# Kernel optimization log

Hardware: AMD Instinct MI355X
Metric: run time of the kernel (lower is better)

Reference implementation:

```python
import jax, jax.numpy as jnp
import numpy as np


def setup_inputs() -> dict:
    key = jax.random.key(0)
    k1, k2 = jax.random.split(key)
    B, S, H = 8, 2048, 1024
    lstm_output = jax.random.normal(k1, (B, S, H), dtype=jnp.float32)
    # xavier-uniform-like init for the bilinear weight
    limit = float(np.sqrt(6.0 / (H + H)))
    attention_weights = jax.random.uniform(k2, (H, H), dtype=jnp.float32, minval=-limit, maxval=limit)
    return {"lstm_output": lstm_output, "attention_weights": attention_weights}


def reference(lstm_output, attention_weights):
    # scores[b,i,j] = (x[b,i] @ W) . x[b,j]
    xw = jnp.einsum('bsh,hk->bsk', lstm_output, attention_weights)      # [B,S,H]
    scores = jnp.einsum('bsk,btk->bst', xw, lstm_output)                # [B,S,S]
    attn = jax.nn.softmax(scores, axis=-1)                              # [B,S,S]
    context = jnp.einsum('bst,bth->bsh', attn, lstm_output)             # [B,S,H]
    return (context, attn)
```

## Files before the change

kernel.cpp:

```cpp
#include <hip/hip_runtime.h>
#include <hip/hip_bf16.h>


#define BB 8
#define SS 2048
#define HH 1024

typedef __attribute__((ext_vector_type(8))) short bf16x8;
typedef __attribute__((ext_vector_type(4))) float f32x4;

__device__ __forceinline__ void async_load16(const void* gsrc, void* ldst) {
    typedef const unsigned int __attribute__((address_space(1)))* gp_t;
    typedef unsigned int __attribute__((address_space(3)))* lp_t;
    __builtin_amdgcn_global_load_lds((gp_t)gsrc, (lp_t)ldst, 16, 0, 0);
}

__device__ __forceinline__ unsigned short f2b(float f) {
    __hip_bfloat16 h = __float2bfloat16(f);
    return *(unsigned short*)&h;
}
__device__ __forceinline__ float b2f(unsigned short u) {
    __hip_bfloat16 h = *(__hip_bfloat16*)&u;
    return __bfloat162float(h);
}

__global__ __launch_bounds__(256) void split_x(const float* __restrict__ X,
                                               unsigned short* __restrict__ Xh,
                                               unsigned short* __restrict__ Xl) {
    const size_t i = ((size_t)blockIdx.x * 256 + threadIdx.x) * 8;
    float4 a = *(const float4*)(X + i);
    float4 b = *(const float4*)(X + i + 4);
    ushort4 h0, h1, l0, l1;
    float v, hf;
    v = a.x; h0.x = f2b(v); hf = b2f(h0.x); l0.x = f2b(v - hf);
    v = a.y; h0.y = f2b(v); hf = b2f(h0.y); l0.y = f2b(v - hf);
    v = a.z; h0.z = f2b(v); hf = b2f(h0.z); l0.z = f2b(v - hf);
    v = a.w; h0.w = f2b(v); hf = b2f(h0.w); l0.w = f2b(v - hf);
    v = b.x; h1.x = f2b(v); hf = b2f(h1.x); l1.x = f2b(v - hf);
    v = b.y; h1.y = f2b(v); hf = b2f(h1.y); l1.y = f2b(v - hf);
    v = b.z; h1.z = f2b(v); hf = b2f(h1.z); l1.z = f2b(v - hf);
    v = b.w; h1.w = f2b(v); hf = b2f(h1.w); l1.w = f2b(v - hf);
    *(ushort4*)(Xh + i) = h0; *(ushort4*)(Xh + i + 4) = h1;
    *(ushort4*)(Xl + i) = l0; *(ushort4*)(Xl + i + 4) = l1;
}

__global__ __launch_bounds__(256) void split_wT(const float* __restrict__ W,
                                                unsigned short* __restrict__ Th,
                                                unsigned short* __restrict__ Tl) {
    const int k0 = blockIdx.y * 64, n0 = blockIdx.x * 64;
    __shared__ float tile[64][65];
#pragma unroll
    for (int q = 0; q < 16; q++) {
        int idx = q * 256 + threadIdx.x;
        int r = idx >> 6, c = idx & 63;
        tile[r][c] = W[(size_t)(k0 + r) * HH + n0 + c];
    }
    __syncthreads();
#pragma unroll
    for (int q = 0; q < 16; q++) {
        int idx = q * 256 + threadIdx.x;
        int r = idx >> 6, c = idx & 63;
        float v = tile[c][r];
        unsigned short h = f2b(v);
        Th[(size_t)(n0 + r) * HH + k0 + c] = h;
        Tl[(size_t)(n0 + r) * HH + k0 + c] = f2b(v - b2f(h));
    }
}

#define SPLIT3_8P_BODY(A_h, A_l, B_h, B_l)                                          \
    __shared__ __align__(16) unsigned short lds[65536];                             \
    const int tid = threadIdx.x;                                                    \
    const int wave = tid >> 6, lane = tid & 63;                                     \
    const int m16 = lane & 15, quad = lane >> 4;                                    \
    const int wy = wave >> 2, wx = wave & 3;                                        \
    const int rP = tid >> 2;                                                        \
    const int kq = (tid & 3) ^ ((rP >> 1) & 3);                                     \
    const int cs = quad ^ ((m16 >> 1) & 3);                                         \
    const int wt16 = wave * 1024;                                                   \
    const int rowA_off = (rP & 63) + ((rP >> 6) << 7);                              \
    const int rowB_off = ((rP >> 5) << 6) + (rP & 31);                              \
    const size_t aOff = (size_t)(i0 + rowA_off) * HH + kq * 8;                      \
    const size_t bOff = (size_t)(j0 + rowB_off) * HH + kq * 8;                      \
    f32x4 acc[2][4][2][2] = {};                                                     \
    bf16x8 a_h[4], a_l[4], b_h[2][2], b_l[2][2];                                    \
    STG_A(0, 0, 0); STG_A(1, 0, 0);                                                 \
    STG_B(0, 0, 0); STG_B(1, 0, 0);                                                 \
    STG_B(0, 1, 1); STG_B(1, 1, 1);                                                 \
    asm volatile("s_waitcnt vmcnt(4)" ::: "memory");                                \
    __builtin_amdgcn_s_barrier();                                                   \
    RD_A(0, 0); RD_B(0, 0); RD_B(1, 0);                                             \
    for (int kt = 0; kt < 32; ++kt) {                                               \
        const int bufc = kt & 1, bufn = bufc ^ 1;                                   \
        const int ktA = kt < 31 ? kt + 1 : 31;                                      \
        const int ktB = kt < 30 ? kt + 2 : 31;                                      \
                                                            \
        STG_A(0, ktA, bufn);                                                        \
        __builtin_amdgcn_s_barrier();                                               \
        __builtin_amdgcn_sched_barrier(0);                                          \
        MFMA_PH(0, 0)                                                               \
        __builtin_amdgcn_sched_barrier(0);                                          \
        __builtin_amdgcn_s_barrier();                                               \
                                                            \
        asm volatile("s_waitcnt vmcnt(6)" ::: "memory");                            \
        STG_A(1, ktA, bufn);                                                        \
        __builtin_amdgcn_s_barrier();                                               \
        __builtin_amdgcn_sched_barrier(0);                                          \
        MFMA_PH(0, 1)                                                               \
        __builtin_amdgcn_sched_barrier(0);                                          \
        RD_A(1, bufc);                                                              \
        __builtin_amdgcn_s_barrier();                                               \
                                                            \
        asm volatile("s_waitcnt vmcnt(6)" ::: "memory");                            \
        STG_B(0, ktB, bufc);                                                        \
        __builtin_amdgcn_s_barrier();                                               \
        __builtin_amdgcn_sched_barrier(0);                                          \
        MFMA_PH(1, 0)                                                               \
        __builtin_amdgcn_sched_barrier(0);                                          \
        RD_B(0, bufn);                                                              \
        __builtin_amdgcn_s_barrier();                                               \
                                                            \
        asm volatile("s_waitcnt vmcnt(4)" ::: "memory");                            \
        STG_B(1, ktB, bufc);                                                        \
        __builtin_amdgcn_s_barrier();                                               \
        __builtin_amdgcn_sched_barrier(0);                                          \
        MFMA_PH(1, 1)                                                               \
        __builtin_amdgcn_sched_barrier(0);                                          \
        RD_B(1, bufn);                                                              \
        RD_A(0, bufn);                                                              \
        __builtin_amdgcn_s_barrier();                                               \
    }

#define STG_A(mh, kt, buf) do { \
        const size_t o_ = aOff + (size_t)(mh) * 64 * HH + (size_t)(kt) * 32; \
        async_load16(A_h + o_, (char*)lds + ((buf) * 32768 + (mh) * 4096) * 2 + wt16); \
        async_load16(A_l + o_, (char*)lds + ((buf) * 32768 + 8192 + (mh) * 4096) * 2 + wt16); \
    } while (0)
#define STG_B(nh, kt, buf) do { \
        const size_t o_ = bOff + (size_t)(nh) * 32 * HH + (size_t)(kt) * 32; \
        async_load16(B_h + o_, (char*)lds + ((buf) * 32768 + 16384 + (nh) * 4096) * 2 + wt16); \
        async_load16(B_l + o_, (char*)lds + ((buf) * 32768 + 24576 + (nh) * 4096) * 2 + wt16); \
    } while (0)
#define RD_A(mh, buf) do { \
        const int s0_ = (buf) * 32768 + ((mh) * 128 + wy * 64 + m16) * 32 + cs * 8; \
        _Pragma("unroll") for (int mi = 0; mi < 4; ++mi) { \
            a_h[mi] = *(const bf16x8*)&lds[s0_ + mi * 512]; \
            a_l[mi] = *(const bf16x8*)&lds[8192 + s0_ + mi * 512]; \
        } } while (0)
#define RD_B(nh, buf) do { \
        const int s0_ = (buf) * 32768 + ((nh) * 128 + wx * 32 + m16) * 32 + cs * 8; \
        _Pragma("unroll") for (int nj = 0; nj < 2; ++nj) { \
            b_h[nh][nj] = *(const bf16x8*)&lds[16384 + s0_ + nj * 512]; \
            b_l[nh][nj] = *(const bf16x8*)&lds[24576 + s0_ + nj * 512]; \
        } } while (0)
#define MFMA_PH(mh, nh) \
        __builtin_amdgcn_s_setprio(1); \
        _Pragma("unroll") for (int mi = 0; mi < 4; ++mi) \
        _Pragma("unroll") for (int nj = 0; nj < 2; ++nj) { \
            acc[mh][mi][nh][nj] = __builtin_amdgcn_mfma_f32_16x16x32_bf16(a_h[mi], b_h[nh][nj], acc[mh][mi][nh][nj], 0, 0, 0); \
            acc[mh][mi][nh][nj] = __builtin_amdgcn_mfma_f32_16x16x32_bf16(a_h[mi], b_l[nh][nj], acc[mh][mi][nh][nj], 0, 0, 0); \
            acc[mh][mi][nh][nj] = __builtin_amdgcn_mfma_f32_16x16x32_bf16(a_l[mi], b_h[nh][nj], acc[mh][mi][nh][nj], 0, 0, 0); \
        } \
        __builtin_amdgcn_s_setprio(0);

__global__ __launch_bounds__(512, 2) void gemm_xw3_8p(const unsigned short* __restrict__ Ah,
                                                      const unsigned short* __restrict__ Al,
                                                      const unsigned short* __restrict__ Bh,
                                                      const unsigned short* __restrict__ Bl,
                                                      unsigned short* __restrict__ Ch,
                                                      unsigned short* __restrict__ Cl) {
    const int b = blockIdx.z;
    const int i0 = blockIdx.y * 256, j0 = blockIdx.x * 256;
    const unsigned short* A_h = Ah + (size_t)b * SS * HH;
    const unsigned short* A_l = Al + (size_t)b * SS * HH;
    const unsigned short* B_h = Bh;
    const unsigned short* B_l = Bl;

    SPLIT3_8P_BODY(A_h, A_l, B_h, B_l)

    unsigned short* ChB = Ch + (size_t)b * SS * HH;
    unsigned short* ClB = Cl + (size_t)b * SS * HH;
#pragma unroll
    for (int mh = 0; mh < 2; ++mh)
#pragma unroll
        for (int mi = 0; mi < 4; ++mi)
#pragma unroll
            for (int nh = 0; nh < 2; ++nh)
#pragma unroll
                for (int nj = 0; nj < 2; ++nj) {
                    const int row = i0 + wy * 128 + mh * 64 + mi * 16 + quad * 4;
                    const int col = j0 + wx * 64 + nh * 32 + nj * 16 + m16;
#pragma unroll
                    for (int reg = 0; reg < 4; ++reg) {
                        float v = acc[mh][mi][nh][nj][reg];
                        unsigned short h = f2b(v);
                        ChB[(size_t)(row + reg) * HH + col] = h;
                        ClB[(size_t)(row + reg) * HH + col] = f2b(v - b2f(h));
                    }
                }
}

__global__ __launch_bounds__(512, 2) void gemm_sc3_8p(const unsigned short* __restrict__ Ah,
                                                      const unsigned short* __restrict__ Al,
                                                      const unsigned short* __restrict__ Bh,
                                                      const unsigned short* __restrict__ Bl,
                                                      float* __restrict__ SC) {
    const int b = blockIdx.z;
    const int i0 = blockIdx.y * 256, j0 = blockIdx.x * 256;
    const unsigned short* A_h = Ah + (size_t)b * SS * HH;
    const unsigned short* A_l = Al + (size_t)b * SS * HH;
    const unsigned short* B_h = Bh + (size_t)b * SS * HH;
    const unsigned short* B_l = Bl + (size_t)b * SS * HH;

    SPLIT3_8P_BODY(A_h, A_l, B_h, B_l)

    float* Cb = SC + (size_t)b * SS * SS;
#pragma unroll
    for (int mh = 0; mh < 2; ++mh)
#pragma unroll
        for (int mi = 0; mi < 4; ++mi)
#pragma unroll
            for (int nh = 0; nh < 2; ++nh)
#pragma unroll
                for (int nj = 0; nj < 2; ++nj) {
                    const int row = i0 + wy * 128 + mh * 64 + mi * 16 + quad * 4;
                    const int col = j0 + wx * 64 + nh * 32 + nj * 16 + m16;
#pragma unroll
                    for (int reg = 0; reg < 4; ++reg)
                        Cb[(size_t)(row + reg) * SS + col] = acc[mh][mi][nh][nj][reg];
                }
}

#undef STG_A
#undef STG_B
#undef RD_A
#undef RD_B
#undef MFMA_PH
#undef SPLIT3_8P_BODY

__global__ __launch_bounds__(256) void softmax_rows(float* __restrict__ P,
                                                    unsigned short* __restrict__ Pb) {
    const size_t row = blockIdx.x;
    float4* p4 = (float4*)(P + row * SS);
    const int tid = threadIdx.x;
    float4 v0 = p4[tid], v1 = p4[tid + 256];
    float m = fmaxf(fmaxf(fmaxf(v0.x, v0.y), fmaxf(v0.z, v0.w)),
                    fmaxf(fmaxf(v1.x, v1.y), fmaxf(v1.z, v1.w)));
#pragma unroll
    for (int off = 32; off; off >>= 1) m = fmaxf(m, __shfl_xor(m, off));
    __shared__ float red[4];
    const int wid = tid >> 6, lane = tid & 63;
    if (lane == 0) red[wid] = m;
    __syncthreads();
    m = fmaxf(fmaxf(red[0], red[1]), fmaxf(red[2], red[3]));
    v0.x = __expf(v0.x - m); v0.y = __expf(v0.y - m);
    v0.z = __expf(v0.z - m); v0.w = __expf(v0.w - m);
    v1.x = __expf(v1.x - m); v1.y = __expf(v1.y - m);
    v1.z = __expf(v1.z - m); v1.w = __expf(v1.w - m);
    float s = v0.x + v0.y + v0.z + v0.w + v1.x + v1.y + v1.z + v1.w;
#pragma unroll
    for (int off = 32; off; off >>= 1) s += __shfl_xor(s, off);
    __syncthreads();
    if (lane == 0) red[wid] = s;
    __syncthreads();
    s = red[0] + red[1] + red[2] + red[3];
    const float inv = 1.0f / s;
    v0.x *= inv; v0.y *= inv; v0.z *= inv; v0.w *= inv;
    v1.x *= inv; v1.y *= inv; v1.z *= inv; v1.w *= inv;
    p4[tid] = v0;
    p4[tid + 256] = v1;
    ushort4* b4 = (ushort4*)(Pb + row * SS);
    ushort4 u0 = { f2b(v0.x), f2b(v0.y), f2b(v0.z), f2b(v0.w) };
    ushort4 u1 = { f2b(v1.x), f2b(v1.y), f2b(v1.z), f2b(v1.w) };
    b4[tid] = u0;
    b4[tid + 256] = u1;
}

__global__ __launch_bounds__(256) void transpose_cvt(const float* __restrict__ X,
                                                     unsigned short* __restrict__ XT) {
    const int b = blockIdx.z;
    const int t0 = blockIdx.y * 64;
    const int h0 = blockIdx.x * 64;
    __shared__ float tile[64][65];
    const float* Xb = X + (size_t)b * SS * HH;
    unsigned short* Tb = XT + (size_t)b * HH * SS;
#pragma unroll
    for (int q = 0; q < 16; q++) {
        int idx = q * 256 + threadIdx.x;
        int r = idx >> 6, c = idx & 63;
        tile[r][c] = Xb[(size_t)(t0 + r) * HH + h0 + c];
    }
    __syncthreads();
#pragma unroll
    for (int q = 0; q < 16; q++) {
        int idx = q * 256 + threadIdx.x;
        int r = idx >> 6, c = idx & 63;
        Tb[(size_t)(h0 + r) * SS + t0 + c] = f2b(tile[c][r]);
    }
}

__global__ __launch_bounds__(512, 2) void gemm_ctx_8p(const unsigned short* __restrict__ Ab,
                                                      const unsigned short* __restrict__ Bt,
                                                      float* __restrict__ C) {
    const int b = blockIdx.z;
    const int i0 = blockIdx.y * 256, n0 = blockIdx.x * 256;
    const unsigned short* A = Ab + (size_t)b * SS * SS;
    const unsigned short* B = Bt + (size_t)b * HH * SS;

    __shared__ __align__(16) unsigned short lds[65536];

    const int tid = threadIdx.x;
    const int wave = tid >> 6, lane = tid & 63;
    const int m16 = lane & 15, quad = lane >> 4;
    const int m7 = m16 & 7;
    const int wy = wave >> 2, wx = wave & 3;
    const int rA8 = tid >> 3;
    const int c8 = (tid & 7) ^ (rA8 & 7);
    const int wt16 = wave * 1024;
    const int sl0 = (quad ^ m7) * 8;
    const int sl1 = ((quad + 4) ^ m7) * 8;

    const size_t aSrc = (size_t)(i0 + rA8) * SS + c8 * 8;
    const size_t bSrc = (size_t)(n0 + ((rA8 >> 5) << 6) + (rA8 & 31)) * SS + c8 * 8;

    f32x4 acc[2][4][2][2] = {};
    bf16x8 a[4][2], bb[2][2][2];

#define CSTG_A(mh, h, kt, buf) \
    async_load16(A + aSrc + (size_t)((mh) * 64 + (h) * 128) * SS + (size_t)(kt) * 64, \
                 (char*)lds + (buf) * 65536 + (mh) * 16384 + (h) * 8192 + wt16)
#define CSTG_B(nh, h, kt, buf) \
    async_load16(B + bSrc + (size_t)((h) * 128 + (nh) * 32) * SS + (size_t)(kt) * 64, \
                 (char*)lds + (buf) * 65536 + 32768 + (nh) * 16384 + (h) * 8192 + wt16)
#define CRD_A(mh, buf) do { \
        const int r0_ = (buf) * 32768 + ((mh) * 128 + wy * 64 + m16) * 64; \
        _Pragma("unroll") for (int mi = 0; mi < 4; ++mi) { \
            a[mi][0] = *(const bf16x8*)&lds[r0_ + mi * 1024 + sl0]; \
            a[mi][1] = *(const bf16x8*)&lds[r0_ + mi * 1024 + sl1]; \
        } } while (0)
#define CRD_B(nh, buf) do { \
        const int r0_ = (buf) * 32768 + 16384 + (nh) * 8192 + (wx * 32 + m16) * 64; \
        _Pragma("unroll") for (int nj = 0; nj < 2; ++nj) { \
            bb[nh][nj][0] = *(const bf16x8*)&lds[r0_ + nj * 1024 + sl0]; \
            bb[nh][nj][1] = *(const bf16x8*)&lds[r0_ + nj * 1024 + sl1]; \
        } } while (0)
#define CMFMA(mh, nh) \
        __builtin_amdgcn_s_setprio(1); \
        _Pragma("unroll") for (int mi = 0; mi < 4; ++mi) \
        _Pragma("unroll") for (int nj = 0; nj < 2; ++nj) { \
            acc[mh][mi][nh][nj] = __builtin_amdgcn_mfma_f32_16x16x32_bf16(a[mi][0], bb[nh][nj][0], acc[mh][mi][nh][nj], 0, 0, 0); \
            acc[mh][mi][nh][nj] = __builtin_amdgcn_mfma_f32_16x16x32_bf16(a[mi][1], bb[nh][nj][1], acc[mh][mi][nh][nj], 0, 0, 0); \
        } \
        __builtin_amdgcn_s_setprio(0);

    CSTG_A(0, 0, 0, 0); CSTG_A(0, 1, 0, 0);
    CSTG_A(1, 0, 0, 0); CSTG_A(1, 1, 0, 0);
    CSTG_B(0, 0, 0, 0); CSTG_B(0, 1, 0, 0);
    CSTG_B(1, 0, 0, 0); CSTG_B(1, 1, 0, 0);
    CSTG_B(0, 0, 1, 1); CSTG_B(0, 1, 1, 1);
    CSTG_B(1, 0, 1, 1); CSTG_B(1, 1, 1, 1);
    asm volatile("s_waitcnt vmcnt(4)" ::: "memory");
    __builtin_amdgcn_s_barrier();
    CRD_A(0, 0); CRD_B(0, 0); CRD_B(1, 0);

    for (int kt = 0; kt < 32; ++kt) {
        const int bufc = kt & 1, bufn = bufc ^ 1;
        const int ktA = kt < 31 ? kt + 1 : 31;
        const int ktB = kt < 30 ? kt + 2 : 31;
        CSTG_A(0, 0, ktA, bufn); CSTG_A(0, 1, ktA, bufn);
        __builtin_amdgcn_s_barrier();
        __builtin_amdgcn_sched_barrier(0);
        CMFMA(0, 0)
        __builtin_amdgcn_sched_barrier(0);
        __builtin_amdgcn_s_barrier();
        asm volatile("s_waitcnt vmcnt(6)" ::: "memory");
        CSTG_A(1, 0, ktA, bufn); CSTG_A(1, 1, ktA, bufn);
        __builtin_amdgcn_s_barrier();
        __builtin_amdgcn_sched_barrier(0);
        CMFMA(0, 1)
        __builtin_amdgcn_sched_barrier(0);
        CRD_A(1, bufc);
        __builtin_amdgcn_s_barrier();
        asm volatile("s_waitcnt vmcnt(6)" ::: "memory");
        CSTG_B(0, 0, ktB, bufc); CSTG_B(0, 1, ktB, bufc);
        __builtin_amdgcn_s_barrier();
        __builtin_amdgcn_sched_barrier(0);
        CMFMA(1, 0)
        __builtin_amdgcn_sched_barrier(0);
        CRD_B(0, bufn);
        __builtin_amdgcn_s_barrier();
        asm volatile("s_waitcnt vmcnt(4)" ::: "memory");
        CSTG_B(1, 0, ktB, bufc); CSTG_B(1, 1, ktB, bufc);
        __builtin_amdgcn_s_barrier();
        __builtin_amdgcn_sched_barrier(0);
        CMFMA(1, 1)
        __builtin_amdgcn_sched_barrier(0);
        CRD_B(1, bufn);
        CRD_A(0, bufn);
        __builtin_amdgcn_s_barrier();
    }

    float* Cb = C + (size_t)b * SS * HH;
#pragma unroll
    for (int mh = 0; mh < 2; ++mh)
#pragma unroll
        for (int mi = 0; mi < 4; ++mi)
#pragma unroll
            for (int nh = 0; nh < 2; ++nh)
#pragma unroll
                for (int nj = 0; nj < 2; ++nj) {
                    const int row = i0 + wy * 128 + mh * 64 + mi * 16 + quad * 4;
                    const int col = n0 + wx * 64 + nh * 32 + nj * 16 + m16;
#pragma unroll
                    for (int reg = 0; reg < 4; ++reg)
                        Cb[(size_t)(row + reg) * HH + col] = acc[mh][mi][nh][nj][reg];
                }
#undef CSTG_A
#undef CSTG_B
#undef CRD_A
#undef CRD_B
#undef CMFMA
}

extern "C" void kernel_launch(void* const* d_in, const int* in_sizes, int n_in,
                              void* d_out, int out_size, void* d_ws, size_t ws_size,
                              hipStream_t stream) {
    const float* X = (const float*)d_in[0];
    const float* W = (const float*)d_in[1];
    float* ctx  = (float*)d_out;
    float* attn = ctx + (size_t)BB * SS * HH;

    char* ws = (char*)d_ws;
    unsigned short* x_hi  = (unsigned short*)ws;
    unsigned short* x_lo  = (unsigned short*)(ws + ((size_t)32 << 20));
    unsigned short* wt_hi = (unsigned short*)(ws + ((size_t)64 << 20));
    unsigned short* wt_lo = (unsigned short*)(ws + ((size_t)66 << 20));
    unsigned short* xT     = x_hi;
    unsigned short* attn_b = x_lo;

    unsigned short* xw_hi = (unsigned short*)d_out;
    unsigned short* xw_lo = xw_hi + (size_t)BB * SS * HH;

    dim3 blk(256);
    split_x <<<dim3(BB * SS * HH / (8 * 256)), blk, 0, stream>>>(X, x_hi, x_lo);
    split_wT<<<dim3(HH / 64, HH / 64), blk, 0, stream>>>(W, wt_hi, wt_lo);
    gemm_xw3_8p<<<dim3(HH / 256, SS / 256, BB), dim3(512), 0, stream>>>(x_hi, x_lo, wt_hi, wt_lo, xw_hi, xw_lo);
    gemm_sc3_8p<<<dim3(SS / 256, SS / 256, BB), dim3(512), 0, stream>>>(xw_hi, xw_lo, x_hi, x_lo, attn);
    transpose_cvt<<<dim3(HH / 64, SS / 64, BB), blk, 0, stream>>>(X, xT);
    softmax_rows <<<dim3(BB * SS), blk, 0, stream>>>(attn, attn_b);
    gemm_ctx_8p<<<dim3(HH / 256, SS / 256, BB), dim3(512), 0, stream>>>(attn_b, xT, ctx);
}
```

Baseline: 602.5 us.

## Merge four-phase MFMA pipeline into two phases with fewer barriers

Restructures the main K-loop of the split-bf16 GEMM kernels and the context GEMM from four MFMA phases per K-step to two. Each phase now issues both halves of the global-to-LDS async loads and runs twice as many MFMAs, which halves the number of s_barrier synchronizations per iteration. The vmcnt wait thresholds are adjusted to match. Cost: larger MFMA bursts with less interleaving of loads and LDS reads, which can expose memory latency.

```diff
diff --git a/kernel.cpp b/kernel.cpp
--- a/kernel.cpp
+++ b/kernel.cpp
@@ -67,7 +67,7 @@
     }
 }
 
-#define SPLIT3_8P_BODY(A_h, A_l, B_h, B_l)                                          \
+#define SPLIT3_2PH_BODY(A_h, A_l, B_h, B_l)                                         \
     __shared__ __align__(16) unsigned short lds[65536];                             \
     const int tid = threadIdx.x;                                                    \
     const int wave = tid >> 6, lane = tid & 63;                                     \
@@ -93,38 +93,25 @@
         const int bufc = kt & 1, bufn = bufc ^ 1;                                   \
         const int ktA = kt < 31 ? kt + 1 : 31;                                      \
         const int ktB = kt < 30 ? kt + 2 : 31;                                      \
-                                                            \
+                                                       \
         STG_A(0, ktA, bufn);                                                        \
+        STG_A(1, ktA, bufn);                                                        \
+        asm volatile("s_waitcnt vmcnt(8)" ::: "memory");                            \
         __builtin_amdgcn_s_barrier();                                               \
         __builtin_amdgcn_sched_barrier(0);                                          \
-        MFMA_PH(0, 0)                                                               \
-        __builtin_amdgcn_sched_barrier(0);                                          \
-        __builtin_amdgcn_s_barrier();                                               \
-                                                            \
-        asm volatile("s_waitcnt vmcnt(6)" ::: "memory");                            \
-        STG_A(1, ktA, bufn);                                                        \
-        __builtin_amdgcn_s_barrier();                                               \
-        __builtin_amdgcn_sched_barrier(0);                                          \
-        MFMA_PH(0, 1)                                                               \
+        MFMA_PH(0)                                                                  \
         __builtin_amdgcn_sched_barrier(0);                                          \
         RD_A(1, bufc);                                                              \
         __builtin_amdgcn_s_barrier();                                               \
-                                                            \
-        asm volatile("s_waitcnt vmcnt(6)" ::: "memory");                            \
+                                                       \
         STG_B(0, ktB, bufc);                                                        \
+        STG_B(1, ktB, bufc);                                                        \
+        asm volatile("s_waitcnt vmcnt(4)" ::: "memory");                            \
         __builtin_amdgcn_s_barrier();                                               \
         __builtin_amdgcn_sched_barrier(0);                                          \
-        MFMA_PH(1, 0)                                                               \
+        MFMA_PH(1)                                                                  \
         __builtin_amdgcn_sched_barrier(0);                                          \
         RD_B(0, bufn);                                                              \
-        __builtin_amdgcn_s_barrier();                                               \
-                                                            \
-        asm volatile("s_waitcnt vmcnt(4)" ::: "memory");                            \
-        STG_B(1, ktB, bufc);                                                        \
-        __builtin_amdgcn_s_barrier();                                               \
-        __builtin_amdgcn_sched_barrier(0);                                          \
-        MFMA_PH(1, 1)                                                               \
-        __builtin_amdgcn_sched_barrier(0);                                          \
         RD_B(1, bufn);                                                              \
         RD_A(0, bufn);                                                              \
         __builtin_amdgcn_s_barrier();                                               \
@@ -152,9 +139,10 @@
             b_h[nh][nj] = *(const bf16x8*)&lds[16384 + s0_ + nj * 512]; \
             b_l[nh][nj] = *(const bf16x8*)&lds[24576 + s0_ + nj * 512]; \
         } } while (0)
-#define MFMA_PH(mh, nh) \
+#define MFMA_PH(mh) \
         __builtin_amdgcn_s_setprio(1); \
         _Pragma("unroll") for (int mi = 0; mi < 4; ++mi) \
+        _Pragma("unroll") for (int nh = 0; nh < 2; ++nh) \
         _Pragma("unroll") for (int nj = 0; nj < 2; ++nj) { \
             acc[mh][mi][nh][nj] = __builtin_amdgcn_mfma_f32_16x16x32_bf16(a_h[mi], b_h[nh][nj], acc[mh][mi][nh][nj], 0, 0, 0); \
             acc[mh][mi][nh][nj] = __builtin_amdgcn_mfma_f32_16x16x32_bf16(a_h[mi], b_l[nh][nj], acc[mh][mi][nh][nj], 0, 0, 0); \
@@ -175,7 +163,7 @@
     const unsigned short* B_h = Bh;
     const unsigned short* B_l = Bl;
 
-    SPLIT3_8P_BODY(A_h, A_l, B_h, B_l)
+    SPLIT3_2PH_BODY(A_h, A_l, B_h, B_l)
 
     unsigned short* ChB = Ch + (size_t)b * SS * HH;
     unsigned short* ClB = Cl + (size_t)b * SS * HH;
@@ -211,7 +199,7 @@
     const unsigned short* B_h = Bh + (size_t)b * SS * HH;
     const unsigned short* B_l = Bl + (size_t)b * SS * HH;
 
-    SPLIT3_8P_BODY(A_h, A_l, B_h, B_l)
+    SPLIT3_2PH_BODY(A_h, A_l, B_h, B_l)
 
     float* Cb = SC + (size_t)b * SS * SS;
 #pragma unroll
@@ -235,7 +223,7 @@
 #undef RD_A
 #undef RD_B
 #undef MFMA_PH
-#undef SPLIT3_8P_BODY
+#undef SPLIT3_2PH_BODY
 
 __global__ __launch_bounds__(256) void softmax_rows(float* __restrict__ P,
                                                     unsigned short* __restrict__ Pb) {
@@ -343,9 +331,10 @@
             bb[nh][nj][0] = *(const bf16x8*)&lds[r0_ + nj * 1024 + sl0]; \
             bb[nh][nj][1] = *(const bf16x8*)&lds[r0_ + nj * 1024 + sl1]; \
         } } while (0)
-#define CMFMA(mh, nh) \
+#define CMFMA(mh) \
         __builtin_amdgcn_s_setprio(1); \
         _Pragma("unroll") for (int mi = 0; mi < 4; ++mi) \
+        _Pragma("unroll") for (int nh = 0; nh < 2; ++nh) \
         _Pragma("unroll") for (int nj = 0; nj < 2; ++nj) { \
             acc[mh][mi][nh][nj] = __builtin_amdgcn_mfma_f32_16x16x32_bf16(a[mi][0], bb[nh][nj][0], acc[mh][mi][nh][nj], 0, 0, 0); \
             acc[mh][mi][nh][nj] = __builtin_amdgcn_mfma_f32_16x16x32_bf16(a[mi][1], bb[nh][nj][1], acc[mh][mi][nh][nj], 0, 0, 0); \
@@ -367,33 +356,22 @@
         const int ktA = kt < 31 ? kt + 1 : 31;
         const int ktB = kt < 30 ? kt + 2 : 31;
         CSTG_A(0, 0, ktA, bufn); CSTG_A(0, 1, ktA, bufn);
+        CSTG_A(1, 0, ktA, bufn); CSTG_A(1, 1, ktA, bufn);
+        asm volatile("s_waitcnt vmcnt(8)" ::: "memory");
         __builtin_amdgcn_s_barrier();
         __builtin_amdgcn_sched_barrier(0);
-        CMFMA(0, 0)
-        __builtin_amdgcn_sched_barrier(0);
-        __builtin_amdgcn_s_barrier();
-        asm volatile("s_waitcnt vmcnt(6)" ::: "memory");
-        CSTG_A(1, 0, ktA, bufn); CSTG_A(1, 1, ktA, bufn);
-        __builtin_amdgcn_s_barrier();
-        __builtin_amdgcn_sched_barrier(0);
-        CMFMA(0, 1)
+        CMFMA(0)
         __builtin_amdgcn_sched_barrier(0);
         CRD_A(1, bufc);
         __builtin_amdgcn_s_barrier();
-        asm volatile("s_waitcnt vmcnt(6)" ::: "memory");
         CSTG_B(0, 0, ktB, bufc); CSTG_B(0, 1, ktB, bufc);
+        CSTG_B(1, 0, ktB, bufc); CSTG_B(1, 1, ktB, bufc);
+        asm volatile("s_waitcnt vmcnt(4)" ::: "memory");
         __builtin_amdgcn_s_barrier();
         __builtin_amdgcn_sched_barrier(0);
-        CMFMA(1, 0)
+        CMFMA(1)
         __builtin_amdgcn_sched_barrier(0);
         CRD_B(0, bufn);
-        __builtin_amdgcn_s_barrier();
-        asm volatile("s_waitcnt vmcnt(4)" ::: "memory");
-        CSTG_B(1, 0, ktB, bufc); CSTG_B(1, 1, ktB, bufc);
-        __builtin_amdgcn_s_barrier();
-        __builtin_amdgcn_sched_barrier(0);
-        CMFMA(1, 1)
-        __builtin_amdgcn_sched_barrier(0);
         CRD_B(1, bufn);
         CRD_A(0, bufn);
         __builtin_amdgcn_s_barrier();
```

Result: no change. 609.5 us (+1.2%).
